# Optimization experiments

Hardware: AMD Instinct MI355X
Metric: run time of the kernel (lower is better)

Reference implementation:

```python
import jax, jax.numpy as jnp
import numpy as np

EPS = 1e-12  # keras K.l2_normalize epsilon


def _l2_normalize(v, axis):
    return v * jax.lax.rsqrt(jnp.maximum(jnp.sum(v * v, axis=axis, keepdims=True), EPS))


def setup_inputs() -> dict:
    key = jax.random.key(0)
    k1, k2, k3, k4 = jax.random.split(key, 4)
    B, T, D, K, O = 32, 1024, 512, 64, 1024
    x = jax.random.normal(k1, (B, T, D), dtype=jnp.float32)
    weight = jax.random.normal(k2, (D, K), dtype=jnp.float32) * (1.0 / np.sqrt(D))
    bias = jnp.zeros((K,), dtype=jnp.float32)
    centers = jax.random.normal(k3, (K, D), dtype=jnp.float32)
    reduc_dim = jax.random.normal(k4, (D * K, O), dtype=jnp.float32) * 0.01
    return {"x": x, "weight": weight, "bias": bias, "centers": centers, "reduc_dim": reduc_dim}


def reference(x, weight, bias, centers, reduc_dim):
    # x: [B,T,D], weight: [D,K], bias: [K]
    # soft assignment: softmax over centers
    a = jax.nn.softmax(jnp.einsum('btd,dk->btk', x, weight) + bias, axis=-1)  # [B,T,K]
    # aggregate descriptors per center: batch_dot over time axis -> [B,K,D]
    x_agg = jnp.einsum('btk,btd->bkd', a, x)
    # total soft weight per center: [B,K]
    sum_w = jnp.sum(a, axis=1)
    # residual vs centers, broadcast: [B,K,D]
    full = x_agg - sum_w[:, :, None] * centers[None, :, :]
    # intra-normalize per center vector
    full = _l2_normalize(full, axis=-1)
    B = x.shape[0]
    full = full.reshape(B, -1)  # [B, K*D]
    full = _l2_normalize(full, axis=-1)
    return full @ reduc_dim  # [B, output_dim]
```

## Files before the change

kernel.cpp:

```cpp
#include <hip/hip_runtime.h>
#include <math.h>

#define TT 1024
#define DD 512
#define KK 64
#define OO 1024
#define EPSF 1e-12f

typedef __attribute__((ext_vector_type(8))) short bf16x8;
typedef __attribute__((ext_vector_type(4))) float f32x4;

__device__ __forceinline__ ushort f2bf(float f) {
  unsigned u = __float_as_uint(f);
  u = (u + 0x7FFFu + ((u >> 16) & 1u)) >> 16;
  return (ushort)u;
}
__device__ __forceinline__ float bf2f(ushort h) {
  unsigned u = ((unsigned)h) << 16;
  return __uint_as_float(u);
}


__global__ void nv_kzero(float* __restrict__ p) {
  p[blockIdx.x * 256 + threadIdx.x] = 0.f;
}

__global__ __launch_bounds__(256) void nv_k0w(const float* __restrict__ w,
                                              ushort* __restrict__ whT) {
  int idx = blockIdx.x * 256 + threadIdx.x;
  int d = idx >> 6, k = idx & 63;
  whT[(size_t)k * DD + d] = f2bf(w[idx]);
}

__global__ __launch_bounds__(256) void nv_k1(
    const float* __restrict__ x, const ushort* __restrict__ whT,
    const float* __restrict__ bias, ushort* __restrict__ aT,
    float* __restrict__ sum_w) {
  const int b = blockIdx.y, t0 = blockIdx.x * 128;
  const int tid = threadIdx.x;
  const int wave = tid >> 6, lane = tid & 63, l15 = lane & 15, q = lane >> 4;

  __shared__ ushort xs[128 * 64];
  __shared__ ushort wsm[64 * 64];

  f32x4 acc[2][4];
#pragma unroll
  for (int mt = 0; mt < 2; ++mt)
#pragma unroll
    for (int nt = 0; nt < 4; ++nt)
#pragma unroll
      for (int r = 0; r < 4; ++r) acc[mt][nt][r] = 0.f;

  for (int dc = 0; dc < DD; dc += 64) {
    __syncthreads();
#pragma unroll
    for (int it = 0; it < 4; ++it) {
      int gid = it * 256 + tid;
      int t = gid >> 3, g = gid & 7;
      const float* px = x + ((size_t)(b * TT + t0 + t) * DD + dc + g * 8);
      float4 v0 = *(const float4*)px;
      float4 v1 = *(const float4*)(px + 4);
      bf16x8 pk;
      pk[0] = (short)f2bf(v0.x); pk[1] = (short)f2bf(v0.y);
      pk[2] = (short)f2bf(v0.z); pk[3] = (short)f2bf(v0.w);
      pk[4] = (short)f2bf(v1.x); pk[5] = (short)f2bf(v1.y);
      pk[6] = (short)f2bf(v1.z); pk[7] = (short)f2bf(v1.w);
      *(bf16x8*)(xs + t * 64 + ((g ^ (t & 7)) << 3)) = pk;
    }
#pragma unroll
    for (int it = 0; it < 2; ++it) {
      int gid = it * 256 + tid;
      int k = gid >> 3, g = gid & 7;
      bf16x8 v = *(const bf16x8*)(whT + (size_t)k * DD + dc + g * 8);
      *(bf16x8*)(wsm + k * 64 + ((g ^ (k & 7)) << 3)) = v;
    }
    __syncthreads();
#pragma unroll
    for (int kc = 0; kc < 2; ++kc) {
      int gq = kc * 4 + q;
      bf16x8 bf[4];
#pragma unroll
      for (int nt = 0; nt < 4; ++nt) {
        int k = nt * 16 + l15;
        bf[nt] = *(const bf16x8*)(wsm + k * 64 + ((gq ^ (k & 7)) << 3));
      }
#pragma unroll
      for (int mt = 0; mt < 2; ++mt) {
        int t = wave * 32 + mt * 16 + l15;
        bf16x8 af = *(const bf16x8*)(xs + t * 64 + ((gq ^ (t & 7)) << 3));
#pragma unroll
        for (int nt = 0; nt < 4; ++nt)
          acc[mt][nt] = __builtin_amdgcn_mfma_f32_16x16x32_bf16(af, bf[nt], acc[mt][nt], 0, 0, 0);
      }
    }
  }

  float bia[4];
#pragma unroll
  for (int nt = 0; nt < 4; ++nt) bia[nt] = bias[nt * 16 + l15];

  ushort au[2][4][4];
  float sw[4] = {0.f, 0.f, 0.f, 0.f};
#pragma unroll
  for (int mt = 0; mt < 2; ++mt)
#pragma unroll
    for (int r = 0; r < 4; ++r) {
      float l[4];
#pragma unroll
      for (int nt = 0; nt < 4; ++nt) l[nt] = acc[mt][nt][r] + bia[nt];
      float m = fmaxf(fmaxf(l[0], l[1]), fmaxf(l[2], l[3]));
#pragma unroll
      for (int s = 1; s <= 8; s <<= 1) m = fmaxf(m, __shfl_xor(m, s));
      float e[4];
#pragma unroll
      for (int nt = 0; nt < 4; ++nt) e[nt] = __expf(l[nt] - m);
      float ssum = e[0] + e[1] + e[2] + e[3];
#pragma unroll
      for (int s = 1; s <= 8; s <<= 1) ssum += __shfl_xor(ssum, s);
      float inv = 1.f / ssum;
#pragma unroll
      for (int nt = 0; nt < 4; ++nt) {
        ushort u = f2bf(e[nt] * inv);
        au[mt][nt][r] = u;
        sw[nt] += bf2f(u);
      }
    }
#pragma unroll
  for (int nt = 0; nt < 4; ++nt) {
    float s = sw[nt];
    s += __shfl_xor(s, 16);
    s += __shfl_xor(s, 32);
    if (q == 0) atomicAdd(sum_w + b * KK + nt * 16 + l15, s);
  }
  __syncthreads();
#pragma unroll
  for (int mt = 0; mt < 2; ++mt)
#pragma unroll
    for (int nt = 0; nt < 4; ++nt)
#pragma unroll
      for (int r = 0; r < 4; ++r) {
        int k = nt * 16 + l15;
        int t = wave * 32 + mt * 16 + q * 4 + r;
        int tg = t >> 3;
        xs[k * 128 + ((tg ^ l15) << 3) + (t & 7)] = au[mt][nt][r];
      }
  __syncthreads();
#pragma unroll
  for (int it = 0; it < 4; ++it) {
    int gid = it * 256 + tid;
    int k = gid >> 4, g = gid & 15;
    bf16x8 v = *(const bf16x8*)(xs + k * 128 + ((g ^ (k & 15)) << 3));
    *(bf16x8*)(aT + (size_t)(b * KK + k) * TT + t0 + g * 8) = v;
  }
}

__global__ __launch_bounds__(256) void nv_k2(
    const ushort* __restrict__ aT, const float* __restrict__ x,
    float* __restrict__ xaggP) {
  const int dsp = blockIdx.x;
  const int b = blockIdx.y;
  const int tsp = blockIdx.z;
  const int tid = threadIdx.x;
  const int wave = tid >> 6, lane = tid & 63, l15 = lane & 15, q = lane >> 4;
  const int d0 = dsp * 64;

  __shared__ ushort asx[64 * 64];
  __shared__ ushort xsT[64 * 64];

  f32x4 acc[4];
#pragma unroll
  for (int nt = 0; nt < 4; ++nt)
#pragma unroll
    for (int r = 0; r < 4; ++r) acc[nt][r] = 0.f;

  for (int tc = 0; tc < 8; ++tc) {
    const int t0 = tsp * 512 + tc * 64;
    __syncthreads();
#pragma unroll
    for (int it = 0; it < 2; ++it) {
      int gid = it * 256 + tid;
      int k = gid >> 3, g = gid & 7;
      bf16x8 v = *(const bf16x8*)(aT + (size_t)(b * KK + k) * TT + t0 + g * 8);
      *(bf16x8*)(asx + k * 64 + ((g ^ (k & 7)) << 3)) = v;
    }
#pragma unroll
    for (int it = 0; it < 4; ++it) {
      int fid = it * 256 + tid;
      int t = fid >> 4, dq = fid & 15;
      float4 v = *(const float4*)(x + (size_t)(b * TT + t0 + t) * DD + d0 + dq * 4);
      int tg = t >> 3;
      float vv[4] = {v.x, v.y, v.z, v.w};
#pragma unroll
      for (int i = 0; i < 4; ++i) {
        int d = dq * 4 + i;
        int pos = tg ^ ((d ^ (d >> 3)) & 7);
        xsT[d * 64 + (pos << 3) + (t & 7)] = f2bf(vv[i]);
      }
    }
    __syncthreads();
#pragma unroll
    for (int kc = 0; kc < 2; ++kc) {
      int gq = kc * 4 + q;
      int k = wave * 16 + l15;
      bf16x8 af = *(const bf16x8*)(asx + k * 64 + ((gq ^ (k & 7)) << 3));
#pragma unroll
      for (int nt = 0; nt < 4; ++nt) {
        int d = nt * 16 + l15;
        int pos = gq ^ ((d ^ (d >> 3)) & 7);
        bf16x8 bf = *(const bf16x8*)(xsT + d * 64 + (pos << 3));
        acc[nt] = __builtin_amdgcn_mfma_f32_16x16x32_bf16(af, bf, acc[nt], 0, 0, 0);
      }
    }
  }
#pragma unroll
  for (int nt = 0; nt < 4; ++nt)
#pragma unroll
    for (int r = 0; r < 4; ++r) {
      int k = wave * 16 + q * 4 + r;
      xaggP[(size_t)((tsp * 32 + b) * KK + k) * DD + d0 + nt * 16 + l15] = acc[nt][r];
    }
}

__global__ __launch_bounds__(128) void nv_k3a(
    const float* __restrict__ xaggP, float* __restrict__ full,
    const float* __restrict__ centers, const float* __restrict__ sum_w,
    float* __restrict__ s1) {
  const int k = blockIdx.x, b = blockIdx.y;
  const int tid = threadIdx.x;
  const float sw = sum_w[b * KK + k];
  float4 v = make_float4(0.f, 0.f, 0.f, 0.f);
#pragma unroll
  for (int sp = 0; sp < 2; ++sp) {
    float4 p = *((const float4*)(xaggP + (size_t)((sp * 32 + b) * KK + k) * DD) + tid);
    v.x += p.x; v.y += p.y; v.z += p.z; v.w += p.w;
  }
  float4 c = *((const float4*)(centers + (size_t)k * DD) + tid);
  v.x = fmaf(-sw, c.x, v.x);
  v.y = fmaf(-sw, c.y, v.y);
  v.z = fmaf(-sw, c.z, v.z);
  v.w = fmaf(-sw, c.w, v.w);
  *((float4*)(full + (size_t)(b * KK + k) * DD) + tid) = v;
  float ss = v.x * v.x + v.y * v.y + v.z * v.z + v.w * v.w;
#pragma unroll
  for (int s = 1; s <= 32; s <<= 1) ss += __shfl_xor(ss, s);
  __shared__ float red[2];
  if ((tid & 63) == 0) red[tid >> 6] = ss;
  __syncthreads();
  if (tid == 0) s1[b * KK + k] = red[0] + red[1];
}

__global__ __launch_bounds__(64) void nv_k3b(const float* __restrict__ s1,
                                             float* __restrict__ scale) {
  const int b = blockIdx.x, k = threadIdx.x;
  float r = s1[b * KK + k];
  float d1 = fmaxf(r, EPSF);
  float s2 = r / d1;
#pragma unroll
  for (int s = 1; s <= 32; s <<= 1) s2 += __shfl_xor(s2, s);
  scale[b * KK + k] = rsqrtf(d1) * rsqrtf(fmaxf(s2, EPSF));
}

__global__ __launch_bounds__(128) void nv_k3c(float* __restrict__ full,
                                              const float* __restrict__ scale) {
  const int blk = blockIdx.x;
  const float sc = scale[blk];
  float4* p = (float4*)(full + (size_t)blk * DD) + threadIdx.x;
  float4 v = *p;
  v.x *= sc; v.y *= sc; v.z *= sc; v.w *= sc;
  *p = v;
}

__global__ __launch_bounds__(256) void nv_k4(
    const float* __restrict__ full, const float* __restrict__ reduc,
    float* __restrict__ outP) {
  const int c_base = blockIdx.x * 64;
  const int r_base = blockIdx.y * 512;
  const int tid = threadIdx.x;
  const int tx = tid & 15;
  const int ty = (tid >> 4) & 3;
  const int tz = tid >> 6;
  const int c0 = c_base + tx * 4;

  __shared__ float As[32 * 256];

  float acc[8][4] = {};

  for (int ch = 0; ch < 2; ++ch) {
    const int rch = r_base + ch * 256;
    __syncthreads();
#pragma unroll
    for (int it = 0; it < 8; ++it) {
      int f4 = it * 256 + tid;
      int bb = f4 >> 6, rr4 = (f4 & 63) << 2;
      *(float4*)(As + bb * 256 + rr4) =
          *(const float4*)(full + (size_t)bb * 32768 + rch + rr4);
    }
    __syncthreads();
#pragma unroll 4
    for (int i = 0; i < 16; ++i) {
      const int rl = i * 16 + ty * 4;
      float wv[4][4];
#pragma unroll
      for (int j = 0; j < 4; ++j) {
        float4 w = *(const float4*)(reduc + (size_t)(rch + rl + j) * OO + c0);
        wv[j][0] = w.x; wv[j][1] = w.y; wv[j][2] = w.z; wv[j][3] = w.w;
      }
#pragma unroll
      for (int bb = 0; bb < 8; ++bb) {
        float4 a4 = *(const float4*)(As + (tz * 8 + bb) * 256 + rl);
        float a_[4] = {a4.x, a4.y, a4.z, a4.w};
#pragma unroll
        for (int j = 0; j < 4; ++j) {
          acc[bb][0] = fmaf(a_[j], wv[j][0], acc[bb][0]);
          acc[bb][1] = fmaf(a_[j], wv[j][1], acc[bb][1]);
          acc[bb][2] = fmaf(a_[j], wv[j][2], acc[bb][2]);
          acc[bb][3] = fmaf(a_[j], wv[j][3], acc[bb][3]);
        }
      }
    }
  }

#pragma unroll
  for (int bb = 0; bb < 8; ++bb) {
    float4 v = make_float4(acc[bb][0], acc[bb][1], acc[bb][2], acc[bb][3]);
    v.x += __shfl_xor(v.x, 16); v.x += __shfl_xor(v.x, 32);
    v.y += __shfl_xor(v.y, 16); v.y += __shfl_xor(v.y, 32);
    v.z += __shfl_xor(v.z, 16); v.z += __shfl_xor(v.z, 32);
    v.w += __shfl_xor(v.w, 16); v.w += __shfl_xor(v.w, 32);
    if (ty == 0) {
      *(float4*)(outP + (size_t)(blockIdx.y * 32 + tz * 8 + bb) * OO + c0) = v;
    }
  }
}

__global__ __launch_bounds__(256) void nv_k5(const float* __restrict__ outP,
                                             float* __restrict__ out) {
  const int idx = blockIdx.x * 256 + threadIdx.x;
  float s = 0.f;
#pragma unroll 8
  for (int sp = 0; sp < 64; ++sp) s += outP[(size_t)sp * 32768 + idx];
  out[idx] = s;
}

extern "C" void kernel_launch(void* const* d_in, const int* in_sizes, int n_in,
                              void* d_out, int out_size, void* d_ws, size_t ws_size,
                              hipStream_t stream) {
  const float* x = (const float*)d_in[0];
  const float* weight = (const float*)d_in[1];
  const float* bias = (const float*)d_in[2];
  const float* centers = (const float*)d_in[3];
  const float* reduc = (const float*)d_in[4];
  float* out = (float*)d_out;
  float* ws = (float*)d_ws;

  ushort* aT = (ushort*)ws;
  float* full = ws + 1048576;
  float* xaggP = ws + 2097152;
  float* outP = ws + 4194304;
  ushort* whT = (ushort*)(ws + 6291456);
  float* sum_w = ws + 6291456 + 16384;
  float* s1 = sum_w + 2048;
  float* scale = sum_w + 4096;

  nv_kzero<<<8, 256, 0, stream>>>(sum_w);
  nv_k0w<<<128, 256, 0, stream>>>(weight, whT);
  nv_k1<<<dim3(8, 32), 256, 0, stream>>>(x, whT, bias, aT, sum_w);
  nv_k2<<<dim3(8, 32, 2), 256, 0, stream>>>(aT, x, xaggP);
  nv_k3a<<<dim3(64, 32), 128, 0, stream>>>(xaggP, full, centers, sum_w, s1);
  nv_k3b<<<32, 64, 0, stream>>>(s1, scale);
  nv_k3c<<<2048, 128, 0, stream>>>(full, scale);
  nv_k4<<<dim3(16, 64), 256, 0, stream>>>(full, reduc, outP);
  nv_k5<<<128, 256, 0, stream>>>(outP, out);
}
```

Baseline: 291.3 us.

## Emit transposed bf16 x from softmax kernel and feed aggregation from it

```diff
diff --git a/kernel.cpp b/kernel.cpp
--- a/kernel.cpp
+++ b/kernel.cpp
@@ -16,82 +16,90 @@
   return (ushort)u;
 }
 __device__ __forceinline__ float bf2f(ushort h) {
-  unsigned u = ((unsigned)h) << 16;
-  return __uint_as_float(u);
-}
-
-
-__global__ void nv_kzero(float* __restrict__ p) {
-  p[blockIdx.x * 256 + threadIdx.x] = 0.f;
-}
-
-__global__ __launch_bounds__(256) void nv_k0w(const float* __restrict__ w,
-                                              ushort* __restrict__ whT) {
+  return __uint_as_float(((unsigned)h) << 16);
+}
+
+
+__global__ __launch_bounds__(256) void nv_k0(const float* __restrict__ w,
+                                             ushort* __restrict__ whT,
+                                             float* __restrict__ sum_w) {
   int idx = blockIdx.x * 256 + threadIdx.x;
-  int d = idx >> 6, k = idx & 63;
-  whT[(size_t)k * DD + d] = f2bf(w[idx]);
+  if (idx < 32768) {
+    int d = idx >> 6, k = idx & 63;
+    whT[(size_t)k * DD + d] = f2bf(w[idx]);
+  } else if (idx < 32768 + 2048) {
+    sum_w[idx - 32768] = 0.f;
+  }
 }
 
 __global__ __launch_bounds__(256) void nv_k1(
     const float* __restrict__ x, const ushort* __restrict__ whT,
     const float* __restrict__ bias, ushort* __restrict__ aT,
-    float* __restrict__ sum_w) {
-  const int b = blockIdx.y, t0 = blockIdx.x * 128;
+    ushort* __restrict__ xbfT, float* __restrict__ sum_w) {
+  const int b = blockIdx.y, t0 = blockIdx.x * 64;
   const int tid = threadIdx.x;
   const int wave = tid >> 6, lane = tid & 63, l15 = lane & 15, q = lane >> 4;
 
-  __shared__ ushort xs[128 * 64];
+  __shared__ ushort xs[64 * 64];
+  __shared__ ushort xsT[64 * 64];
   __shared__ ushort wsm[64 * 64];
 
-  f32x4 acc[2][4];
-#pragma unroll
-  for (int mt = 0; mt < 2; ++mt)
-#pragma unroll
-    for (int nt = 0; nt < 4; ++nt)
-#pragma unroll
-      for (int r = 0; r < 4; ++r) acc[mt][nt][r] = 0.f;
+  f32x4 acc[4];
+#pragma unroll
+  for (int nt = 0; nt < 4; ++nt)
+#pragma unroll
+    for (int r = 0; r < 4; ++r) acc[nt][r] = 0.f;
 
   for (int dc = 0; dc < DD; dc += 64) {
     __syncthreads();
 #pragma unroll
-    for (int it = 0; it < 4; ++it) {
-      int gid = it * 256 + tid;
-      int t = gid >> 3, g = gid & 7;
-      const float* px = x + ((size_t)(b * TT + t0 + t) * DD + dc + g * 8);
+    for (int it = 0; it < 2; ++it) {
+      int gi = it * 256 + tid;
+      int t = gi >> 3, gd = gi & 7;
+      const float* px = x + (size_t)(b * TT + t0 + t) * DD + dc + gd * 8;
       float4 v0 = *(const float4*)px;
       float4 v1 = *(const float4*)(px + 4);
+      ushort u[8];
+      u[0] = f2bf(v0.x); u[1] = f2bf(v0.y); u[2] = f2bf(v0.z); u[3] = f2bf(v0.w);
+      u[4] = f2bf(v1.x); u[5] = f2bf(v1.y); u[6] = f2bf(v1.z); u[7] = f2bf(v1.w);
       bf16x8 pk;
-      pk[0] = (short)f2bf(v0.x); pk[1] = (short)f2bf(v0.y);
-      pk[2] = (short)f2bf(v0.z); pk[3] = (short)f2bf(v0.w);
-      pk[4] = (short)f2bf(v1.x); pk[5] = (short)f2bf(v1.y);
-      pk[6] = (short)f2bf(v1.z); pk[7] = (short)f2bf(v1.w);
-      *(bf16x8*)(xs + t * 64 + ((g ^ (t & 7)) << 3)) = pk;
-    }
-#pragma unroll
-    for (int it = 0; it < 2; ++it) {
-      int gid = it * 256 + tid;
-      int k = gid >> 3, g = gid & 7;
-      bf16x8 v = *(const bf16x8*)(whT + (size_t)k * DD + dc + g * 8);
-      *(bf16x8*)(wsm + k * 64 + ((g ^ (k & 7)) << 3)) = v;
+#pragma unroll
+      for (int i = 0; i < 8; ++i) pk[i] = (short)u[i];
+      *(bf16x8*)(xs + t * 64 + ((gd ^ (t & 7)) << 3)) = pk;
+      int tg = t >> 3;
+#pragma unroll
+      for (int i = 0; i < 8; ++i) {
+        int d = gd * 8 + i;
+        xsT[d * 64 + ((tg ^ ((d >> 3) & 7)) << 3) + (t & 7)] = u[i];
+      }
+    }
+#pragma unroll
+    for (int it = 0; it < 2; ++it) {
+      int gi = it * 256 + tid;
+      int k = gi >> 3, gd = gi & 7;
+      bf16x8 v = *(const bf16x8*)(whT + (size_t)k * DD + dc + gd * 8);
+      *(bf16x8*)(wsm + k * 64 + ((gd ^ (k & 7)) << 3)) = v;
     }
     __syncthreads();
 #pragma unroll
     for (int kc = 0; kc < 2; ++kc) {
       int gq = kc * 4 + q;
-      bf16x8 bf[4];
+      int t = wave * 16 + l15;
+      bf16x8 af = *(const bf16x8*)(xs + t * 64 + ((gq ^ (t & 7)) << 3));
 #pragma unroll
       for (int nt = 0; nt < 4; ++nt) {
         int k = nt * 16 + l15;
-        bf[nt] = *(const bf16x8*)(wsm + k * 64 + ((gq ^ (k & 7)) << 3));
-      }
-#pragma unroll
-      for (int mt = 0; mt < 2; ++mt) {
-        int t = wave * 32 + mt * 16 + l15;
-        bf16x8 af = *(const bf16x8*)(xs + t * 64 + ((gq ^ (t & 7)) << 3));
-#pragma unroll
-        for (int nt = 0; nt < 4; ++nt)
-          acc[mt][nt] = __builtin_amdgcn_mfma_f32_16x16x32_bf16(af, bf[nt], acc[mt][nt], 0, 0, 0);
-      }
+        bf16x8 bfv = *(const bf16x8*)(wsm + k * 64 + ((gq ^ (k & 7)) << 3));
+        acc[nt] = __builtin_amdgcn_mfma_f32_16x16x32_bf16(af, bfv, acc[nt], 0, 0, 0);
+      }
+    }
+#pragma unroll
+    for (int it = 0; it < 2; ++it) {
+      int gi = it * 256 + tid;
+      int d = gi >> 3, g = gi & 7;
+      bf16x8 v = *(const bf16x8*)(xsT + d * 64 + (g << 3));
+      int tg = g ^ ((d >> 3) & 7);
+      *(bf16x8*)(xbfT + (size_t)(b * DD + dc + d) * TT + t0 + tg * 8) = v;
     }
   }
 
@@ -99,32 +107,30 @@
 #pragma unroll
   for (int nt = 0; nt < 4; ++nt) bia[nt] = bias[nt * 16 + l15];
 
-  ushort au[2][4][4];
+  ushort au[4][4];
   float sw[4] = {0.f, 0.f, 0.f, 0.f};
 #pragma unroll
-  for (int mt = 0; mt < 2; ++mt)
-#pragma unroll
-    for (int r = 0; r < 4; ++r) {
-      float l[4];
-#pragma unroll
-      for (int nt = 0; nt < 4; ++nt) l[nt] = acc[mt][nt][r] + bia[nt];
-      float m = fmaxf(fmaxf(l[0], l[1]), fmaxf(l[2], l[3]));
-#pragma unroll
-      for (int s = 1; s <= 8; s <<= 1) m = fmaxf(m, __shfl_xor(m, s));
-      float e[4];
-#pragma unroll
-      for (int nt = 0; nt < 4; ++nt) e[nt] = __expf(l[nt] - m);
-      float ssum = e[0] + e[1] + e[2] + e[3];
-#pragma unroll
-      for (int s = 1; s <= 8; s <<= 1) ssum += __shfl_xor(ssum, s);
-      float inv = 1.f / ssum;
-#pragma unroll
-      for (int nt = 0; nt < 4; ++nt) {
-        ushort u = f2bf(e[nt] * inv);
-        au[mt][nt][r] = u;
-        sw[nt] += bf2f(u);
-      }
-    }
+  for (int r = 0; r < 4; ++r) {
+    float l[4];
+#pragma unroll
+    for (int nt = 0; nt < 4; ++nt) l[nt] = acc[nt][r] + bia[nt];
+    float m = fmaxf(fmaxf(l[0], l[1]), fmaxf(l[2], l[3]));
+#pragma unroll
+    for (int s = 1; s <= 8; s <<= 1) m = fmaxf(m, __shfl_xor(m, s));
+    float e[4];
+#pragma unroll
+    for (int nt = 0; nt < 4; ++nt) e[nt] = __expf(l[nt] - m);
+    float ssum = e[0] + e[1] + e[2] + e[3];
+#pragma unroll
+    for (int s = 1; s <= 8; s <<= 1) ssum += __shfl_xor(ssum, s);
+    float inv = 1.f / ssum;
+#pragma unroll
+    for (int nt = 0; nt < 4; ++nt) {
+      ushort u = f2bf(e[nt] * inv);
+      au[nt][r] = u;
+      sw[nt] += bf2f(u);
+    }
+  }
 #pragma unroll
   for (int nt = 0; nt < 4; ++nt) {
     float s = sw[nt];
@@ -134,38 +140,35 @@
   }
   __syncthreads();
 #pragma unroll
-  for (int mt = 0; mt < 2; ++mt)
-#pragma unroll
-    for (int nt = 0; nt < 4; ++nt)
-#pragma unroll
-      for (int r = 0; r < 4; ++r) {
-        int k = nt * 16 + l15;
-        int t = wave * 32 + mt * 16 + q * 4 + r;
-        int tg = t >> 3;
-        xs[k * 128 + ((tg ^ l15) << 3) + (t & 7)] = au[mt][nt][r];
-      }
+  for (int nt = 0; nt < 4; ++nt)
+#pragma unroll
+    for (int r = 0; r < 4; ++r) {
+      int k = nt * 16 + l15;
+      int t = wave * 16 + q * 4 + r;
+      xs[k * 64 + (((t >> 3) ^ (k & 7)) << 3) + (t & 7)] = au[nt][r];
+    }
   __syncthreads();
 #pragma unroll
-  for (int it = 0; it < 4; ++it) {
-    int gid = it * 256 + tid;
-    int k = gid >> 4, g = gid & 15;
-    bf16x8 v = *(const bf16x8*)(xs + k * 128 + ((g ^ (k & 15)) << 3));
-    *(bf16x8*)(aT + (size_t)(b * KK + k) * TT + t0 + g * 8) = v;
+  for (int it = 0; it < 2; ++it) {
+    int gi = it * 256 + tid;
+    int k = gi >> 3, g = gi & 7;
+    bf16x8 v = *(const bf16x8*)(xs + k * 64 + (g << 3));
+    int tg = g ^ (k & 7);
+    *(bf16x8*)(aT + (size_t)(b * KK + k) * TT + t0 + tg * 8) = v;
   }
 }
 
 __global__ __launch_bounds__(256) void nv_k2(
-    const ushort* __restrict__ aT, const float* __restrict__ x,
+    const ushort* __restrict__ aT, const ushort* __restrict__ xbfT,
     float* __restrict__ xaggP) {
-  const int dsp = blockIdx.x;
+  const int d0 = blockIdx.x * 64;
   const int b = blockIdx.y;
   const int tsp = blockIdx.z;
   const int tid = threadIdx.x;
   const int wave = tid >> 6, lane = tid & 63, l15 = lane & 15, q = lane >> 4;
-  const int d0 = dsp * 64;
 
   __shared__ ushort asx[64 * 64];
-  __shared__ ushort xsT[64 * 64];
+  __shared__ ushort xsb[64 * 64];
 
   f32x4 acc[4];
 #pragma unroll
@@ -173,29 +176,22 @@
 #pragma unroll
     for (int r = 0; r < 4; ++r) acc[nt][r] = 0.f;
 
-  for (int tc = 0; tc < 8; ++tc) {
-    const int t0 = tsp * 512 + tc * 64;
-    __syncthreads();
-#pragma unroll
-    for (int it = 0; it < 2; ++it) {
-      int gid = it * 256 + tid;
-      int k = gid >> 3, g = gid & 7;
+  for (int tc = 0; tc < 4; ++tc) {
+    const int t0 = tsp * 256 + tc * 64;
+    __syncthreads();
+#pragma unroll
+    for (int it = 0; it < 2; ++it) {
+      int gi = it * 256 + tid;
+      int k = gi >> 3, g = gi & 7;
       bf16x8 v = *(const bf16x8*)(aT + (size_t)(b * KK + k) * TT + t0 + g * 8);
       *(bf16x8*)(asx + k * 64 + ((g ^ (k & 7)) << 3)) = v;
     }
 #pragma unroll
-    for (int it = 0; it < 4; ++it) {
-      int fid = it * 256 + tid;
-      int t = fid >> 4, dq = fid & 15;
-      float4 v = *(const float4*)(x + (size_t)(b * TT + t0 + t) * DD + d0 + dq * 4);
-      int tg = t >> 3;
-      float vv[4] = {v.x, v.y, v.z, v.w};
-#pragma unroll
-      for (int i = 0; i < 4; ++i) {
-        int d = dq * 4 + i;
-        int pos = tg ^ ((d ^ (d >> 3)) & 7);
-        xsT[d * 64 + (pos << 3) + (t & 7)] = f2bf(vv[i]);
-      }
+    for (int it = 0; it < 2; ++it) {
+      int gi = it * 256 + tid;
+      int d = gi >> 3, g = gi & 7;
+      bf16x8 v = *(const bf16x8*)(xbfT + (size_t)(b * DD + d0 + d) * TT + t0 + g * 8);
+      *(bf16x8*)(xsb + d * 64 + ((g ^ (d & 7)) << 3)) = v;
     }
     __syncthreads();
 #pragma unroll
@@ -206,9 +202,8 @@
 #pragma unroll
       for (int nt = 0; nt < 4; ++nt) {
         int d = nt * 16 + l15;
-        int pos = gq ^ ((d ^ (d >> 3)) & 7);
-        bf16x8 bf = *(const bf16x8*)(xsT + d * 64 + (pos << 3));
-        acc[nt] = __builtin_amdgcn_mfma_f32_16x16x32_bf16(af, bf, acc[nt], 0, 0, 0);
+        bf16x8 bfv = *(const bf16x8*)(xsb + d * 64 + ((gq ^ (d & 7)) << 3));
+        acc[nt] = __builtin_amdgcn_mfma_f32_16x16x32_bf16(af, bfv, acc[nt], 0, 0, 0);
       }
     }
   }
@@ -230,7 +225,7 @@
   const float sw = sum_w[b * KK + k];
   float4 v = make_float4(0.f, 0.f, 0.f, 0.f);
 #pragma unroll
-  for (int sp = 0; sp < 2; ++sp) {
+  for (int sp = 0; sp < 4; ++sp) {
     float4 p = *((const float4*)(xaggP + (size_t)((sp * 32 + b) * KK + k) * DD) + tid);
     v.x += p.x; v.y += p.y; v.z += p.z; v.w += p.w;
   }
@@ -260,18 +255,20 @@
   scale[b * KK + k] = rsqrtf(d1) * rsqrtf(fmaxf(s2, EPSF));
 }
 
-__global__ __launch_bounds__(128) void nv_k3c(float* __restrict__ full,
-                                              const float* __restrict__ scale) {
+__global__ __launch_bounds__(128) void nv_k3c(const float* __restrict__ full,
+                                              const float* __restrict__ scale,
+                                              ushort* __restrict__ fullbf) {
   const int blk = blockIdx.x;
   const float sc = scale[blk];
-  float4* p = (float4*)(full + (size_t)blk * DD) + threadIdx.x;
-  float4 v = *p;
-  v.x *= sc; v.y *= sc; v.z *= sc; v.w *= sc;
-  *p = v;
+  float4 v = *((const float4*)(full + (size_t)blk * DD) + threadIdx.x);
+  ushort4 o;
+  o.x = f2bf(v.x * sc); o.y = f2bf(v.y * sc);
+  o.z = f2bf(v.z * sc); o.w = f2bf(v.w * sc);
+  *((ushort4*)(fullbf + (size_t)blk * DD) + threadIdx.x) = o;
 }
 
 __global__ __launch_bounds__(256) void nv_k4(
-    const float* __restrict__ full, const float* __restrict__ reduc,
+    const ushort* __restrict__ fullbf, const float* __restrict__ reduc,
     float* __restrict__ outP) {
   const int c_base = blockIdx.x * 64;
   const int r_base = blockIdx.y * 512;
@@ -281,23 +278,29 @@
   const int tz = tid >> 6;
   const int c0 = c_base + tx * 4;
 
-  __shared__ float As[32 * 256];
+  __shared__ float As2[32 * 128];
 
   float acc[8][4] = {};
 
-  for (int ch = 0; ch < 2; ++ch) {
-    const int rch = r_base + ch * 256;
-    __syncthreads();
-#pragma unroll
-    for (int it = 0; it < 8; ++it) {
-      int f4 = it * 256 + tid;
-      int bb = f4 >> 6, rr4 = (f4 & 63) << 2;
-      *(float4*)(As + bb * 256 + rr4) =
-          *(const float4*)(full + (size_t)bb * 32768 + rch + rr4);
+  for (int ch = 0; ch < 4; ++ch) {
+    const int rch = r_base + ch * 128;
+    __syncthreads();
+#pragma unroll
+    for (int it = 0; it < 2; ++it) {
+      int gi = it * 256 + tid;
+      int bb = gi >> 4, g = gi & 15;
+      bf16x8 v = *(const bf16x8*)(fullbf + (size_t)bb * 32768 + rch + g * 8);
+      float4 lo, hi;
+      lo.x = bf2f((ushort)v[0]); lo.y = bf2f((ushort)v[1]);
+      lo.z = bf2f((ushort)v[2]); lo.w = bf2f((ushort)v[3]);
+      hi.x = bf2f((ushort)v[4]); hi.y = bf2f((ushort)v[5]);
+      hi.z = bf2f((ushort)v[6]); hi.w = bf2f((ushort)v[7]);
+      *(float4*)(As2 + bb * 128 + g * 8) = lo;
+      *(float4*)(As2 + bb * 128 + g * 8 + 4) = hi;
     }
     __syncthreads();
 #pragma unroll 4
-    for (int i = 0; i < 16; ++i) {
+    for (int i = 0; i < 8; ++i) {
       const int rl = i * 16 + ty * 4;
       float wv[4][4];
 #pragma unroll
@@ -307,7 +310,7 @@
       }
 #pragma unroll
       for (int bb = 0; bb < 8; ++bb) {
-        float4 a4 = *(const float4*)(As + (tz * 8 + bb) * 256 + rl);
+        float4 a4 = *(const float4*)(As2 + (tz * 8 + bb) * 128 + rl);
         float a_[4] = {a4.x, a4.y, a4.z, a4.w};
 #pragma unroll
         for (int j = 0; j < 4; ++j) {
@@ -354,21 +357,22 @@
   float* ws = (float*)d_ws;
 
   ushort* aT = (ushort*)ws;
-  float* full = ws + 1048576;
-  float* xaggP = ws + 2097152;
-  float* outP = ws + 4194304;
-  ushort* whT = (ushort*)(ws + 6291456);
-  float* sum_w = ws + 6291456 + 16384;
+  ushort* xbfT = (ushort*)(ws + 1048576);
+  float* xaggP = ws + 9437184;
+  float* full = ws + 13631488;
+  ushort* fullbf = (ushort*)(ws + 14680064);
+  float* outP = ws + 15728640;
+  ushort* whT = (ushort*)(ws + 17825792);
+  float* sum_w = ws + 17825792 + 16384;
   float* s1 = sum_w + 2048;
   float* scale = sum_w + 4096;
 
-  nv_kzero<<<8, 256, 0, stream>>>(sum_w);
-  nv_k0w<<<128, 256, 0, stream>>>(weight, whT);
-  nv_k1<<<dim3(8, 32), 256, 0, stream>>>(x, whT, bias, aT, sum_w);
-  nv_k2<<<dim3(8, 32, 2), 256, 0, stream>>>(aT, x, xaggP);
+  nv_k0<<<136, 256, 0, stream>>>(weight, whT, sum_w);
+  nv_k1<<<dim3(16, 32), 256, 0, stream>>>(x, whT, bias, aT, xbfT, sum_w);
+  nv_k2<<<dim3(8, 32, 4), 256, 0, stream>>>(aT, xbfT, xaggP);
   nv_k3a<<<dim3(64, 32), 128, 0, stream>>>(xaggP, full, centers, sum_w, s1);
   nv_k3b<<<32, 64, 0, stream>>>(s1, scale);
-  nv_k3c<<<2048, 128, 0, stream>>>(full, scale);
-  nv_k4<<<dim3(16, 64), 256, 0, stream>>>(full, reduc, outP);
+  nv_k3c<<<2048, 128, 0, stream>>>(full, scale, fullbf);
+  nv_k4<<<dim3(16, 64), 256, 0, stream>>>(fullbf, reduc, outP);
   nv_k5<<<128, 256, 0, stream>>>(outP, out);
 }
```

Result: slower. 319.4 us (+9.7%).
